# Optimization experiments

Measured on AMD Instinct MI355X. Metric: run time of the kernel, lower is better.

The kernel has to match this reference:

```python
import jax, jax.numpy as jnp
import numpy as np

N = 30000   # nodes
E = 600000  # edges
IN = 256    # in_channels
HID = 128   # 2*out_channels
OUT = 64    # out_channels


def setup_inputs() -> dict:
    key = jax.random.key(0)
    k = jax.random.split(key, 6)
    x = jax.random.normal(k[0], (N, IN), dtype=jnp.float32)
    edge_index = jax.random.randint(k[1], (2, E), 0, N, dtype=jnp.int64)
    W1 = jax.random.normal(k[2], (IN, HID), dtype=jnp.float32) * (1.0 / np.sqrt(IN))
    b1 = jnp.zeros((HID,), dtype=jnp.float32)
    W2 = jax.random.normal(k[3], (HID, OUT), dtype=jnp.float32) * (1.0 / np.sqrt(HID))
    b2 = jnp.zeros((OUT,), dtype=jnp.float32)
    return {"x": x, "edge_index": edge_index, "W1": W1, "b1": b1, "W2": W2, "b2": b2}


def _gcn_norm(edge_index, n_nodes):
    # PyG gcn_norm with add_self_loops=True, edge_weight=1
    loop = jnp.arange(n_nodes, dtype=edge_index.dtype)
    src = jnp.concatenate([edge_index[0], loop])
    dst = jnp.concatenate([edge_index[1], loop])
    deg = jax.ops.segment_sum(jnp.ones_like(dst, dtype=jnp.float32), dst,
                              num_segments=n_nodes)
    dinv = jnp.where(deg > 0, jax.lax.rsqrt(deg), 0.0)
    norm = dinv[src] * dinv[dst]  # [E+N]
    return src, dst, norm


def _gcn_conv(h, src, dst, norm, W, b, n_nodes):
    h = h @ W                              # [N, out] linear first (PyG order)
    msg = h[src] * norm[:, None]           # gather + per-edge scale, [E+N, out]
    out = jax.ops.segment_sum(msg, dst, num_segments=n_nodes)  # scatter-add
    return out + b


def reference(x, edge_index, W1, b1, W2, b2):
    n_nodes = x.shape[0]
    src, dst, norm = _gcn_norm(edge_index, n_nodes)
    h = _gcn_conv(x, src, dst, norm, W1, b1, n_nodes)
    h = jax.nn.relu(h)
    return _gcn_conv(h, src, dst, norm, W2, b2, n_nodes)
```

## Files before the change

### kernel.cpp

```cpp
#include <hip/hip_runtime.h>


#define GCN_IN 256
#define GCN_HID 128
#define GCN_OUT 64

#define BKT 128
#define SBE 4096
#define CAP 4096
#define SRCM 0x1FFFFFFu

typedef unsigned short ushort_t;
typedef __attribute__((ext_vector_type(8))) short short8;
typedef __attribute__((ext_vector_type(8))) unsigned short ushort8;
typedef __attribute__((ext_vector_type(4))) float f32x4;

__device__ inline float bf2f(ushort_t u) {
  union { unsigned int i; float f; } x; x.i = ((unsigned int)u) << 16; return x.f;
}
__device__ inline ushort_t f2bf(float f) {
  union { float f; unsigned int i; } u; u.f = f;
  unsigned int r = u.i + 0x7FFFu + ((u.i >> 16) & 1u);
  return (ushort_t)(r >> 16);
}

__global__ __launch_bounds__(256)
void stageX_kernel(const int* __restrict__ ei, int E,
                   int* __restrict__ gcur, int nbin,
                   unsigned int* __restrict__ stage) {
  __shared__ int lcnt[256];
  __shared__ int cur[256];
  __shared__ int nzc;
  const int t = threadIdx.x;
  const int sb = blockIdx.x;
  lcnt[t] = 0;
  if (t == 0) nzc = 0;
  __syncthreads();
  if (t < 128 && ei[2 * t + 1] != 0) atomicAdd(&nzc, 1);
  __syncthreads();
  const bool i64 = (nzc == 0);
  const int base = sb * SBE;
  int end = base + SBE; if (end > E) end = E;

  unsigned int p[16];
  int bk[16];
#pragma unroll
  for (int k = 0; k < 16; ++k) {
    int i = base + t + k * 256;
    bk[k] = -1;
    if (i < end) {
      int s, d;
      if (i64) { s = ei[2 * i]; d = ei[2 * E + 2 * i]; }
      else     { s = ei[i];     d = ei[E + i]; }
      p[k] = (unsigned int)s | ((unsigned int)(d & 127) << 25);
      bk[k] = d >> 7;
      atomicAdd(&lcnt[bk[k]], 1);
    }
  }
  __syncthreads();
  for (int b = t; b < nbin; b += 256) {
    int c = lcnt[b];
    cur[b] = b * CAP + (c ? atomicAdd(&gcur[b], c) : 0);
  }
  __syncthreads();
#pragma unroll
  for (int k = 0; k < 16; ++k) {
    if (bk[k] >= 0) {
      int pos = atomicAdd(&cur[bk[k]], 1);
      if (pos < (bk[k] + 1) * CAP)
        stage[pos] = p[k];
    }
  }
}

__global__ __launch_bounds__(256)
void scatter_kernel(const unsigned int* __restrict__ stage,
                    const int* __restrict__ gcur, int nbin,
                    int* __restrict__ csr_src,
                    int* __restrict__ row_ptr, int* __restrict__ deg,
                    float* __restrict__ dinv, int n) {
  __shared__ int lcnt[BKT];
  __shared__ int lscan[BKT];
  __shared__ int lcur[BKT];
  const int t = threadIdx.x;
  const int b = blockIdx.x;
  const int node0 = b * BKT;
  const int nn = (n - node0 < BKT) ? (n - node0) : BKT;
  const int rb = b * CAP;
  const int re = rb + gcur[b];
  if (t < BKT) lcnt[t] = 0;
  __syncthreads();
  for (int i = rb + t; i < re; i += 256)
    atomicAdd(&lcnt[stage[i] >> 25], 1);
  __syncthreads();
  if (t < BKT) lscan[t] = lcnt[t];
  __syncthreads();
  for (int off = 1; off < BKT; off <<= 1) {
    int v = 0;
    if (t < BKT && t >= off) v = lscan[t - off];
    __syncthreads();
    if (t < BKT) lscan[t] += v;
    __syncthreads();
  }
  if (t < BKT) {
    int excl = rb + lscan[t] - lcnt[t];
    lcur[t] = excl;
    if (t < nn) {
      row_ptr[node0 + t] = excl;
      deg[node0 + t] = lcnt[t];
      dinv[node0 + t] = rsqrtf((float)(lcnt[t] + 1));
    }
  }
  __syncthreads();
  for (int i = rb + t; i < re; i += 256) {
    unsigned int p = stage[i];
    int l = p >> 25;
    int pos = atomicAdd(&lcur[l], 1);
    csr_src[pos] = (int)(p & SRCM);
  }
}

__global__ void prep_w_kernel(const void* __restrict__ W1, const void* __restrict__ W2,
                              ushort_t* __restrict__ Wt1, ushort_t* __restrict__ Wt2,
                              int* __restrict__ flags, int* __restrict__ gcur) {
  __shared__ int csh;
  if (threadIdx.x == 0) csh = 0;
  __syncthreads();
  if (threadIdx.x < 128) {
    ushort_t u = ((const ushort_t*)W1)[2 * threadIdx.x];
    int e = (u >> 7) & 0xFF;
    if (e >= 100 && e <= 140) atomicAdd(&csh, 1);
  }
  __syncthreads();
  bool f32 = (csh < 64);
  if (blockIdx.x == 0) {
    if (threadIdx.x == 0) flags[0] = f32 ? 1 : 0;
    gcur[threadIdx.x] = 0;
  }

  int i = blockIdx.x * blockDim.x + threadIdx.x;
  if (i < GCN_IN * GCN_HID) {
    int k = i >> 7, n = i & 127;
    float v = f32 ? ((const float*)W1)[i] : bf2f(((const ushort_t*)W1)[i]);
    Wt1[n * GCN_IN + k] = f2bf(v);
  }
  int j = i - GCN_IN * GCN_HID;
  if (j >= 0 && j < GCN_HID * GCN_OUT) {
    int k = j >> 6, n = j & 63;
    float v = f32 ? ((const float*)W2)[j] : bf2f(((const ushort_t*)W2)[j]);
    Wt2[n * GCN_HID + k] = f2bf(v);
  }
}

template<int K, int NC, int A_MODE>
__global__ __launch_bounds__(256)
void gemm_mfma_kernel(const void* __restrict__ A, const ushort_t* __restrict__ Bt,
                      ushort_t* __restrict__ C, int M, const int* __restrict__ flags) {
  constexpr int KH = (K > 128) ? 128 : K;
  constexpr int KPC = KH / 8;
  constexpr int NT = NC / 32;
  __shared__ ushort_t As[32 * KH];
  __shared__ ushort_t Bs[NC * KH];
  const int tid = threadIdx.x;
  const int wv = tid >> 6;
  const int lane = tid & 63;
  const int ml = lane & 15;
  const int quad = lane >> 4;
  const int row0 = blockIdx.x * 32;
  const int mrow = (wv & 1) * 16 + ml;
  const int ncol0 = (wv >> 1) * (NC / 2);
  const bool aF32 = (A_MODE == 0) && (flags[0] != 0);
  f32x4 acc[NT] = {};

  for (int ch = 0; ch < K; ch += KH) {
    if (ch) __syncthreads();
    for (int c = tid; c < 32 * KPC; c += 256) {
      int r = c / KPC, cq = c % KPC;
      ushort8 o;
      if (row0 + r < M) {
        if (aF32) {
          const float* ap = (const float*)A + (size_t)(row0 + r) * K + ch + cq * 8;
          float4 f0 = *(const float4*)ap;
          float4 f1 = *(const float4*)(ap + 4);
          o[0] = f2bf(f0.x); o[1] = f2bf(f0.y); o[2] = f2bf(f0.z); o[3] = f2bf(f0.w);
          o[4] = f2bf(f1.x); o[5] = f2bf(f1.y); o[6] = f2bf(f1.z); o[7] = f2bf(f1.w);
        } else {
          o = *(const ushort8*)((const ushort_t*)A + (size_t)(row0 + r) * K + ch + cq * 8);
        }
      } else {
        o = (ushort8)0;
      }
      int byte = (cq * 16) ^ ((r & 7) << 4);
      *(ushort8*)((char*)As + r * (KH * 2) + byte) = o;
    }
    for (int c = tid; c < NC * KPC; c += 256) {
      int nr = c / KPC, cq = c % KPC;
      ushort8 o = *(const ushort8*)(Bt + (size_t)nr * K + ch + cq * 8);
      int byte = (cq * 16) ^ ((nr & 7) << 4);
      *(ushort8*)((char*)Bs + nr * (KH * 2) + byte) = o;
    }
    __syncthreads();
#pragma unroll
    for (int kt = 0; kt < KH; kt += 32) {
      int abyte = (kt * 2 + quad * 16) ^ ((mrow & 7) << 4);
      short8 af = *(const short8*)((const char*)As + mrow * (KH * 2) + abyte);
#pragma unroll
      for (int t = 0; t < NT; ++t) {
        int nr = ncol0 + t * 16 + ml;
        int bbyte = (kt * 2 + quad * 16) ^ ((nr & 7) << 4);
        short8 bf = *(const short8*)((const char*)Bs + nr * (KH * 2) + bbyte);
        acc[t] = __builtin_amdgcn_mfma_f32_16x16x32_bf16(af, bf, acc[t], 0, 0, 0);
      }
    }
  }

  const int orow = row0 + (wv & 1) * 16 + quad * 4;
#pragma unroll
  for (int t = 0; t < NT; ++t) {
    int col = ncol0 + t * 16 + ml;
#pragma unroll
    for (int r = 0; r < 4; ++r) {
      if (orow + r < M)
        C[(size_t)(orow + r) * NC + col] = f2bf(acc[t][r]);
    }
  }
}

__global__ void aggregate_relu_kernel(const ushort_t* __restrict__ h,
                                      const int* __restrict__ row_ptr,
                                      const int* __restrict__ deg,
                                      const int* __restrict__ csr_src,
                                      const float* __restrict__ dinv,
                                      const void* __restrict__ bias,
                                      ushort_t* __restrict__ outp, int n,
                                      const int* __restrict__ flags) {
  const int lane = threadIdx.x & 63;
  const int v = blockIdx.x * 16 + (threadIdx.x >> 4);
  if (v >= n) return;
  const int q = lane & 15;
  const int gb = lane & 48;
  float acc[8] = {};
  const int beg = row_ptr[v];
  const int end = beg + deg[v];
  for (int base = beg; base < end; base += 16) {
    int navail = end - base; if (navail > 16) navail = 16;
    int sv = 0; float dv = 0.f;
    if (base + q < end) { sv = csr_src[base + q]; dv = dinv[sv]; }
    for (int j = 0; j < navail; j += 4) {
      int s0 = __shfl(sv, gb + j + 0), s1 = __shfl(sv, gb + j + 1);
      int s2 = __shfl(sv, gb + j + 2), s3 = __shfl(sv, gb + j + 3);
      float d0 = __shfl(dv, gb + j + 0), d1 = __shfl(dv, gb + j + 1);
      float d2 = __shfl(dv, gb + j + 2), d3 = __shfl(dv, gb + j + 3);
      ushort8 hv0 = *(const ushort8*)(h + (size_t)s0 * GCN_HID + q * 8);
      ushort8 hv1 = *(const ushort8*)(h + (size_t)s1 * GCN_HID + q * 8);
      ushort8 hv2 = *(const ushort8*)(h + (size_t)s2 * GCN_HID + q * 8);
      ushort8 hv3 = *(const ushort8*)(h + (size_t)s3 * GCN_HID + q * 8);
#pragma unroll
      for (int k = 0; k < 8; ++k) {
        acc[k] = fmaf(d0, bf2f(hv0[k]), acc[k]);
        acc[k] = fmaf(d1, bf2f(hv1[k]), acc[k]);
        acc[k] = fmaf(d2, bf2f(hv2[k]), acc[k]);
        acc[k] = fmaf(d3, bf2f(hv3[k]), acc[k]);
      }
    }
  }
  float di = dinv[v];
  float sl = di * di;
  ushort8 hv = *(const ushort8*)(h + (size_t)v * GCN_HID + q * 8);
  const bool bF32 = flags[0] != 0;
  ushort8 o;
#pragma unroll
  for (int k = 0; k < 8; ++k) {
    float bv = bF32 ? ((const float*)bias)[q * 8 + k]
                    : bf2f(((const ushort_t*)bias)[q * 8 + k]);
    o[k] = f2bf(fmaxf(di * acc[k] + sl * bf2f(hv[k]) + bv, 0.f));
  }
  *(ushort8*)(outp + (size_t)v * GCN_HID + q * 8) = o;
}

__global__ void aggregate_out_kernel(const ushort_t* __restrict__ h,
                                     const int* __restrict__ row_ptr,
                                     const int* __restrict__ deg,
                                     const int* __restrict__ csr_src,
                                     const float* __restrict__ dinv,
                                     const void* __restrict__ bias,
                                     void* __restrict__ outp, int n,
                                     const int* __restrict__ flags) {
  const int lane = threadIdx.x & 63;
  const int v = blockIdx.x * 32 + (threadIdx.x >> 3);
  if (v >= n) return;
  const int q = lane & 7;
  const int gb = lane & 56;
  float acc[8] = {};
  const int beg = row_ptr[v];
  const int end = beg + deg[v];
  for (int base = beg; base < end; base += 8) {
    int navail = end - base; if (navail > 8) navail = 8;
    int sv = 0; float dv = 0.f;
    if (base + q < end) { sv = csr_src[base + q]; dv = dinv[sv]; }
    for (int j = 0; j < navail; j += 4) {
      int s0 = __shfl(sv, gb + j + 0), s1 = __shfl(sv, gb + j + 1);
      int s2 = __shfl(sv, gb + j + 2), s3 = __shfl(sv, gb + j + 3);
      float d0 = __shfl(dv, gb + j + 0), d1 = __shfl(dv, gb + j + 1);
      float d2 = __shfl(dv, gb + j + 2), d3 = __shfl(dv, gb + j + 3);
      ushort8 hv0 = *(const ushort8*)(h + (size_t)s0 * GCN_OUT + q * 8);
      ushort8 hv1 = *(const ushort8*)(h + (size_t)s1 * GCN_OUT + q * 8);
      ushort8 hv2 = *(const ushort8*)(h + (size_t)s2 * GCN_OUT + q * 8);
      ushort8 hv3 = *(const ushort8*)(h + (size_t)s3 * GCN_OUT + q * 8);
#pragma unroll
      for (int k = 0; k < 8; ++k) {
        acc[k] = fmaf(d0, bf2f(hv0[k]), acc[k]);
        acc[k] = fmaf(d1, bf2f(hv1[k]), acc[k]);
        acc[k] = fmaf(d2, bf2f(hv2[k]), acc[k]);
        acc[k] = fmaf(d3, bf2f(hv3[k]), acc[k]);
      }
    }
  }
  float di = dinv[v];
  float sl = di * di;
  ushort8 hv = *(const ushort8*)(h + (size_t)v * GCN_OUT + q * 8);
  const bool oF32 = flags[0] != 0;
  float r[8];
#pragma unroll
  for (int k = 0; k < 8; ++k) {
    float bv = oF32 ? ((const float*)bias)[q * 8 + k]
                    : bf2f(((const ushort_t*)bias)[q * 8 + k]);
    r[k] = di * acc[k] + sl * bf2f(hv[k]) + bv;
  }
  if (oF32) {
    float* op = (float*)outp + (size_t)v * GCN_OUT + q * 8;
    *(float4*)op = make_float4(r[0], r[1], r[2], r[3]);
    *(float4*)(op + 4) = make_float4(r[4], r[5], r[6], r[7]);
  } else {
    ushort8 o;
#pragma unroll
    for (int k = 0; k < 8; ++k) o[k] = f2bf(r[k]);
    *(ushort8*)((ushort_t*)outp + (size_t)v * GCN_OUT + q * 8) = o;
  }
}


extern "C" void kernel_launch(void* const* d_in, const int* in_sizes, int n_in,
                              void* d_out, int out_size, void* d_ws, size_t ws_size,
                              hipStream_t stream) {
  const void* x  = d_in[0];
  const int*  ei = (const int*)d_in[1];
  const void* W1 = d_in[2];
  const void* b1 = d_in[3];
  const void* W2 = d_in[4];
  const void* b2 = d_in[5];

  const int N = in_sizes[0] / GCN_IN;
  const int E = in_sizes[1] / 2;
  const int nsb  = (E + SBE - 1) / SBE;
  const int nbin = (N + BKT - 1) / BKT;

  size_t off = 0;
  auto alloc = [&](size_t bytes) -> void* {
    void* p = (char*)d_ws + off;
    off += (bytes + 255) & ~(size_t)255;
    return p;
  };
  int*          flags   = (int*)alloc(256);
  int*          gcur    = (int*)alloc(256 * 4);
  unsigned int* stage   = (unsigned int*)alloc((size_t)nbin * CAP * 4);
  int*          csr_src = (int*)alloc((size_t)nbin * CAP * 4);
  int*          row_ptr = (int*)alloc((size_t)N * 4);
  int*          deg     = (int*)alloc((size_t)N * 4);
  float*        dinv    = (float*)alloc((size_t)N * 4);
  ushort_t*     h1      = (ushort_t*)alloc((size_t)N * GCN_HID * 2);
  ushort_t*     hag     = (ushort_t*)alloc((size_t)N * GCN_HID * 2);
  ushort_t*     wt1     = (ushort_t*)alloc((size_t)GCN_HID * GCN_IN * 2);
  ushort_t*     wt2     = (ushort_t*)alloc((size_t)GCN_OUT * GCN_HID * 2);
  ushort_t*     h2      = h1;

  prep_w_kernel<<<(GCN_IN * GCN_HID + GCN_HID * GCN_OUT + 255) / 256, 256, 0, stream>>>(
      W1, W2, wt1, wt2, flags, gcur);

  stageX_kernel<<<nsb, 256, 0, stream>>>(ei, E, gcur, nbin, stage);
  scatter_kernel<<<nbin, 256, 0, stream>>>(stage, gcur, nbin, csr_src,
                                           row_ptr, deg, dinv, N);

  gemm_mfma_kernel<GCN_IN, GCN_HID, 0>
      <<<(N + 31) / 32, 256, 0, stream>>>(x, wt1, h1, N, flags);

  aggregate_relu_kernel<<<(N + 15) / 16, 256, 0, stream>>>(
      h1, row_ptr, deg, csr_src, dinv, b1, hag, N, flags);

  gemm_mfma_kernel<GCN_HID, GCN_OUT, 2>
      <<<(N + 31) / 32, 256, 0, stream>>>(hag, wt2, h2, N, flags);

  aggregate_out_kernel<<<(N + 31) / 32, 256, 0, stream>>>(
      h2, row_ptr, deg, csr_src, dinv, b2, d_out, N, flags);
}
```

Before: 158.5 us.

## Fuse weight prep, scatter+GEMM1, and aggregation+GEMM2 into fewer kernels

Weight transpose/convert moves into the edge staging kernel, and a memset replaces the gcur reset. The CSR scatter and the first GEMM now run as one launch with block-index dispatch, so they execute concurrently. Layer-1 aggregation is fused with the second GEMM through swizzled LDS tiles, which drops the intermediate hag buffer round-trip and two launches. In exchange, each aggregation block reloads W2 into LDS, the GEMM2 tile shrinks to 16 rows, and occupancy may drop from the larger shared-memory footprint.

```diff
diff --git a/kernel.cpp b/kernel.cpp
--- a/kernel.cpp
+++ b/kernel.cpp
@@ -26,22 +26,46 @@
 
 __global__ __launch_bounds__(256)
 void stageX_kernel(const int* __restrict__ ei, int E,
+                   const void* __restrict__ W1, const void* __restrict__ W2,
+                   ushort_t* __restrict__ Wt1, ushort_t* __restrict__ Wt2,
+                   int* __restrict__ flags,
                    int* __restrict__ gcur, int nbin,
                    unsigned int* __restrict__ stage) {
   __shared__ int lcnt[256];
   __shared__ int cur[256];
-  __shared__ int nzc;
+  __shared__ int nzc, csh;
   const int t = threadIdx.x;
   const int sb = blockIdx.x;
   lcnt[t] = 0;
-  if (t == 0) nzc = 0;
-  __syncthreads();
-  if (t < 128 && ei[2 * t + 1] != 0) atomicAdd(&nzc, 1);
+  if (t == 0) { nzc = 0; csh = 0; }
+  __syncthreads();
+  if (t < 128) {
+    if (ei[2 * t + 1] != 0) atomicAdd(&nzc, 1);
+    ushort_t u = ((const ushort_t*)W1)[2 * t];
+    int e = (u >> 7) & 0xFF;
+    if (e >= 100 && e <= 140) atomicAdd(&csh, 1);
+  }
   __syncthreads();
   const bool i64 = (nzc == 0);
+  const bool f32 = (csh < 64);
+  if (sb == 0 && t == 0) flags[0] = f32 ? 1 : 0;
+
+  for (int i = sb * 256 + t; i < GCN_IN * GCN_HID + GCN_HID * GCN_OUT;
+       i += gridDim.x * 256) {
+    if (i < GCN_IN * GCN_HID) {
+      int k = i >> 7, nn = i & 127;
+      float vv = f32 ? ((const float*)W1)[i] : bf2f(((const ushort_t*)W1)[i]);
+      Wt1[nn * GCN_IN + k] = f2bf(vv);
+    } else {
+      int j = i - GCN_IN * GCN_HID;
+      int k = j >> 6, nn = j & 63;
+      float vv = f32 ? ((const float*)W2)[j] : bf2f(((const ushort_t*)W2)[j]);
+      Wt2[nn * GCN_HID + k] = f2bf(vv);
+    }
+  }
+
   const int base = sb * SBE;
   int end = base + SBE; if (end > E) end = E;
-
   unsigned int p[16];
   int bk[16];
 #pragma unroll
@@ -73,17 +97,16 @@
   }
 }
 
-__global__ __launch_bounds__(256)
-void scatter_kernel(const unsigned int* __restrict__ stage,
-                    const int* __restrict__ gcur, int nbin,
-                    int* __restrict__ csr_src,
-                    int* __restrict__ row_ptr, int* __restrict__ deg,
-                    float* __restrict__ dinv, int n) {
-  __shared__ int lcnt[BKT];
-  __shared__ int lscan[BKT];
-  __shared__ int lcur[BKT];
+__device__ void scatter_body(char* lds,
+                             const unsigned int* __restrict__ stage,
+                             const int* __restrict__ gcur, int nbin,
+                             int* __restrict__ csr_src,
+                             int* __restrict__ row_ptr, int* __restrict__ deg,
+                             float* __restrict__ dinv, int n, int b) {
+  int* lcnt  = (int*)lds;
+  int* lscan = lcnt + BKT;
+  int* lcur  = lcnt + 2 * BKT;
   const int t = threadIdx.x;
-  const int b = blockIdx.x;
   const int node0 = b * BKT;
   const int nn = (n - node0 < BKT) ? (n - node0) : BKT;
   const int rb = b * CAP;
@@ -120,56 +143,25 @@
   }
 }
 
-__global__ void prep_w_kernel(const void* __restrict__ W1, const void* __restrict__ W2,
-                              ushort_t* __restrict__ Wt1, ushort_t* __restrict__ Wt2,
-                              int* __restrict__ flags, int* __restrict__ gcur) {
-  __shared__ int csh;
-  if (threadIdx.x == 0) csh = 0;
-  __syncthreads();
-  if (threadIdx.x < 128) {
-    ushort_t u = ((const ushort_t*)W1)[2 * threadIdx.x];
-    int e = (u >> 7) & 0xFF;
-    if (e >= 100 && e <= 140) atomicAdd(&csh, 1);
-  }
-  __syncthreads();
-  bool f32 = (csh < 64);
-  if (blockIdx.x == 0) {
-    if (threadIdx.x == 0) flags[0] = f32 ? 1 : 0;
-    gcur[threadIdx.x] = 0;
-  }
-
-  int i = blockIdx.x * blockDim.x + threadIdx.x;
-  if (i < GCN_IN * GCN_HID) {
-    int k = i >> 7, n = i & 127;
-    float v = f32 ? ((const float*)W1)[i] : bf2f(((const ushort_t*)W1)[i]);
-    Wt1[n * GCN_IN + k] = f2bf(v);
-  }
-  int j = i - GCN_IN * GCN_HID;
-  if (j >= 0 && j < GCN_HID * GCN_OUT) {
-    int k = j >> 6, n = j & 63;
-    float v = f32 ? ((const float*)W2)[j] : bf2f(((const ushort_t*)W2)[j]);
-    Wt2[n * GCN_HID + k] = f2bf(v);
-  }
-}
-
-template<int K, int NC, int A_MODE>
-__global__ __launch_bounds__(256)
-void gemm_mfma_kernel(const void* __restrict__ A, const ushort_t* __restrict__ Bt,
-                      ushort_t* __restrict__ C, int M, const int* __restrict__ flags) {
-  constexpr int KH = (K > 128) ? 128 : K;
+__device__ void gemm1_body(char* lds, const void* __restrict__ A,
+                           const ushort_t* __restrict__ Bt,
+                           ushort_t* __restrict__ C, int M,
+                           const int* __restrict__ flags, int bid) {
+  constexpr int K = GCN_IN, NC = GCN_HID;
+  constexpr int KH = 128;
   constexpr int KPC = KH / 8;
   constexpr int NT = NC / 32;
-  __shared__ ushort_t As[32 * KH];
-  __shared__ ushort_t Bs[NC * KH];
+  ushort_t* As = (ushort_t*)lds;
+  ushort_t* Bs = As + 32 * KH;
   const int tid = threadIdx.x;
   const int wv = tid >> 6;
   const int lane = tid & 63;
   const int ml = lane & 15;
   const int quad = lane >> 4;
-  const int row0 = blockIdx.x * 32;
+  const int row0 = bid * 32;
   const int mrow = (wv & 1) * 16 + ml;
   const int ncol0 = (wv >> 1) * (NC / 2);
-  const bool aF32 = (A_MODE == 0) && (flags[0] != 0);
+  const bool aF32 = (flags[0] != 0);
   f32x4 acc[NT] = {};
 
   for (int ch = 0; ch < K; ch += KH) {
@@ -226,56 +218,114 @@
   }
 }
 
-__global__ void aggregate_relu_kernel(const ushort_t* __restrict__ h,
-                                      const int* __restrict__ row_ptr,
-                                      const int* __restrict__ deg,
-                                      const int* __restrict__ csr_src,
-                                      const float* __restrict__ dinv,
-                                      const void* __restrict__ bias,
-                                      ushort_t* __restrict__ outp, int n,
-                                      const int* __restrict__ flags) {
-  const int lane = threadIdx.x & 63;
-  const int v = blockIdx.x * 16 + (threadIdx.x >> 4);
-  if (v >= n) return;
+__global__ __launch_bounds__(256)
+void scatter_gemm1_kernel(const unsigned int* __restrict__ stage,
+                          const int* __restrict__ gcur, int nbin,
+                          int* __restrict__ csr_src,
+                          int* __restrict__ row_ptr, int* __restrict__ deg,
+                          float* __restrict__ dinv, int n,
+                          const void* __restrict__ x,
+                          const ushort_t* __restrict__ wt1,
+                          ushort_t* __restrict__ h1,
+                          const int* __restrict__ flags) {
+  __shared__ __align__(16) char lds[32 * 128 * 2 + 128 * 128 * 2];
+  const int b = blockIdx.x;
+  if (b < nbin) {
+    scatter_body(lds, stage, gcur, nbin, csr_src, row_ptr, deg, dinv, n, b);
+  } else {
+    gemm1_body(lds, x, wt1, h1, n, flags, b - nbin);
+  }
+}
+
+__global__ __launch_bounds__(256)
+void agg1_gemm2_kernel(const ushort_t* __restrict__ h,
+                       const int* __restrict__ row_ptr,
+                       const int* __restrict__ deg,
+                       const int* __restrict__ csr_src,
+                       const float* __restrict__ dinv,
+                       const void* __restrict__ bias,
+                       const ushort_t* __restrict__ wt2,
+                       ushort_t* __restrict__ h2, int n,
+                       const int* __restrict__ flags) {
+  __shared__ __align__(16) ushort_t hagS[16 * GCN_HID];
+  __shared__ __align__(16) ushort_t w2S[GCN_OUT * GCN_HID];
+  const int tid = threadIdx.x;
+  const int lane = tid & 63;
+  const int ni = tid >> 4;
+  const int v0 = blockIdx.x * 16;
+  const int v = v0 + ni;
   const int q = lane & 15;
   const int gb = lane & 48;
-  float acc[8] = {};
-  const int beg = row_ptr[v];
-  const int end = beg + deg[v];
-  for (int base = beg; base < end; base += 16) {
-    int navail = end - base; if (navail > 16) navail = 16;
-    int sv = 0; float dv = 0.f;
-    if (base + q < end) { sv = csr_src[base + q]; dv = dinv[sv]; }
-    for (int j = 0; j < navail; j += 4) {
-      int s0 = __shfl(sv, gb + j + 0), s1 = __shfl(sv, gb + j + 1);
-      int s2 = __shfl(sv, gb + j + 2), s3 = __shfl(sv, gb + j + 3);
-      float d0 = __shfl(dv, gb + j + 0), d1 = __shfl(dv, gb + j + 1);
-      float d2 = __shfl(dv, gb + j + 2), d3 = __shfl(dv, gb + j + 3);
-      ushort8 hv0 = *(const ushort8*)(h + (size_t)s0 * GCN_HID + q * 8);
-      ushort8 hv1 = *(const ushort8*)(h + (size_t)s1 * GCN_HID + q * 8);
-      ushort8 hv2 = *(const ushort8*)(h + (size_t)s2 * GCN_HID + q * 8);
-      ushort8 hv3 = *(const ushort8*)(h + (size_t)s3 * GCN_HID + q * 8);
-#pragma unroll
-      for (int k = 0; k < 8; ++k) {
-        acc[k] = fmaf(d0, bf2f(hv0[k]), acc[k]);
-        acc[k] = fmaf(d1, bf2f(hv1[k]), acc[k]);
-        acc[k] = fmaf(d2, bf2f(hv2[k]), acc[k]);
-        acc[k] = fmaf(d3, bf2f(hv3[k]), acc[k]);
+
+  for (int c = tid; c < GCN_OUT * (GCN_HID / 8); c += 256) {
+    int nr = c >> 4, cq = c & 15;
+    ushort8 o = *(const ushort8*)(wt2 + (size_t)nr * GCN_HID + cq * 8);
+    int byte = (cq * 16) ^ ((nr & 7) << 4);
+    *(ushort8*)((char*)w2S + nr * (GCN_HID * 2) + byte) = o;
+  }
+
+  if (v < n) {
+    float acc[8] = {};
+    const int beg = row_ptr[v];
+    const int end = beg + deg[v];
+    for (int base = beg; base < end; base += 16) {
+      int navail = end - base; if (navail > 16) navail = 16;
+      int sv = 0; float dv = 0.f;
+      if (base + q < end) { sv = csr_src[base + q]; dv = dinv[sv]; }
+      for (int j = 0; j < navail; j += 4) {
+        int s0 = __shfl(sv, gb + j + 0), s1 = __shfl(sv, gb + j + 1);
+        int s2 = __shfl(sv, gb + j + 2), s3 = __shfl(sv, gb + j + 3);
+        float d0 = __shfl(dv, gb + j + 0), d1 = __shfl(dv, gb + j + 1);
+        float d2 = __shfl(dv, gb + j + 2), d3 = __shfl(dv, gb + j + 3);
+        ushort8 hv0 = *(const ushort8*)(h + (size_t)s0 * GCN_HID + q * 8);
+        ushort8 hv1 = *(const ushort8*)(h + (size_t)s1 * GCN_HID + q * 8);
+        ushort8 hv2 = *(const ushort8*)(h + (size_t)s2 * GCN_HID + q * 8);
+        ushort8 hv3 = *(const ushort8*)(h + (size_t)s3 * GCN_HID + q * 8);
+#pragma unroll
+        for (int k = 0; k < 8; ++k) {
+          acc[k] = fmaf(d0, bf2f(hv0[k]), acc[k]);
+          acc[k] = fmaf(d1, bf2f(hv1[k]), acc[k]);
+          acc[k] = fmaf(d2, bf2f(hv2[k]), acc[k]);
+          acc[k] = fmaf(d3, bf2f(hv3[k]), acc[k]);
+        }
       }
     }
-  }
-  float di = dinv[v];
-  float sl = di * di;
-  ushort8 hv = *(const ushort8*)(h + (size_t)v * GCN_HID + q * 8);
-  const bool bF32 = flags[0] != 0;
-  ushort8 o;
-#pragma unroll
-  for (int k = 0; k < 8; ++k) {
-    float bv = bF32 ? ((const float*)bias)[q * 8 + k]
-                    : bf2f(((const ushort_t*)bias)[q * 8 + k]);
-    o[k] = f2bf(fmaxf(di * acc[k] + sl * bf2f(hv[k]) + bv, 0.f));
-  }
-  *(ushort8*)(outp + (size_t)v * GCN_HID + q * 8) = o;
+    float di = dinv[v];
+    float sl = di * di;
+    ushort8 hv = *(const ushort8*)(h + (size_t)v * GCN_HID + q * 8);
+    const bool bF32 = flags[0] != 0;
+    ushort8 o;
+#pragma unroll
+    for (int k = 0; k < 8; ++k) {
+      float bv = bF32 ? ((const float*)bias)[q * 8 + k]
+                      : bf2f(((const ushort_t*)bias)[q * 8 + k]);
+      o[k] = f2bf(fmaxf(di * acc[k] + sl * bf2f(hv[k]) + bv, 0.f));
+    }
+    int byte = (q * 16) ^ ((ni & 7) << 4);
+    *(ushort8*)((char*)hagS + ni * (GCN_HID * 2) + byte) = o;
+  }
+  __syncthreads();
+
+  const int wv = tid >> 6;
+  const int ml = lane & 15;
+  const int quad = lane >> 4;
+  f32x4 acc2 = {};
+#pragma unroll
+  for (int kt = 0; kt < GCN_HID; kt += 32) {
+    int abyte = (kt * 2 + quad * 16) ^ ((ml & 7) << 4);
+    short8 af = *(const short8*)((const char*)hagS + ml * (GCN_HID * 2) + abyte);
+    int nr = wv * 16 + ml;
+    int bbyte = (kt * 2 + quad * 16) ^ ((nr & 7) << 4);
+    short8 bf = *(const short8*)((const char*)w2S + nr * (GCN_HID * 2) + bbyte);
+    acc2 = __builtin_amdgcn_mfma_f32_16x16x32_bf16(af, bf, acc2, 0, 0, 0);
+  }
+  const int col = wv * 16 + ml;
+#pragma unroll
+  for (int r = 0; r < 4; ++r) {
+    int row = quad * 4 + r;
+    if (v0 + row < n)
+      h2[(size_t)(v0 + row) * GCN_OUT + col] = f2bf(acc2[r]);
+  }
 }
 
 __global__ void aggregate_out_kernel(const ushort_t* __restrict__ h,
@@ -369,26 +419,21 @@
   int*          deg     = (int*)alloc((size_t)N * 4);
   float*        dinv    = (float*)alloc((size_t)N * 4);
   ushort_t*     h1      = (ushort_t*)alloc((size_t)N * GCN_HID * 2);
-  ushort_t*     hag     = (ushort_t*)alloc((size_t)N * GCN_HID * 2);
+  ushort_t*     h2      = (ushort_t*)alloc((size_t)N * GCN_OUT * 2);
   ushort_t*     wt1     = (ushort_t*)alloc((size_t)GCN_HID * GCN_IN * 2);
   ushort_t*     wt2     = (ushort_t*)alloc((size_t)GCN_OUT * GCN_HID * 2);
-  ushort_t*     h2      = h1;
-
-  prep_w_kernel<<<(GCN_IN * GCN_HID + GCN_HID * GCN_OUT + 255) / 256, 256, 0, stream>>>(
-      W1, W2, wt1, wt2, flags, gcur);
-
-  stageX_kernel<<<nsb, 256, 0, stream>>>(ei, E, gcur, nbin, stage);
-  scatter_kernel<<<nbin, 256, 0, stream>>>(stage, gcur, nbin, csr_src,
-                                           row_ptr, deg, dinv, N);
-
-  gemm_mfma_kernel<GCN_IN, GCN_HID, 0>
-      <<<(N + 31) / 32, 256, 0, stream>>>(x, wt1, h1, N, flags);
-
-  aggregate_relu_kernel<<<(N + 15) / 16, 256, 0, stream>>>(
-      h1, row_ptr, deg, csr_src, dinv, b1, hag, N, flags);
-
-  gemm_mfma_kernel<GCN_HID, GCN_OUT, 2>
-      <<<(N + 31) / 32, 256, 0, stream>>>(hag, wt2, h2, N, flags);
+
+  hipMemsetAsync(gcur, 0, 256 * 4, stream);
+
+  stageX_kernel<<<nsb, 256, 0, stream>>>(ei, E, W1, W2, wt1, wt2, flags,
+                                         gcur, nbin, stage);
+
+  const int nGemm1 = (N + 31) / 32;
+  scatter_gemm1_kernel<<<nbin + nGemm1, 256, 0, stream>>>(
+      stage, gcur, nbin, csr_src, row_ptr, deg, dinv, N, x, wt1, h1, flags);
+
+  agg1_gemm2_kernel<<<(N + 15) / 16, 256, 0, stream>>>(
+      h1, row_ptr, deg, csr_src, dinv, b1, wt2, h2, N, flags);
 
   aggregate_out_kernel<<<(N + 31) / 32, 256, 0, stream>>>(
       h2, row_ptr, deg, csr_src, dinv, b2, d_out, N, flags);
```

Measured after the change: 149.0 us. 1.06x faster.
